# Kernel optimization log

Hardware: AMD Instinct MI355X
Metric: run time of the kernel (lower is better)

## Reference

```python
import jax, jax.numpy as jnp
import numpy as np

LATENT_DIM = 512
IN_CH = 256
OUT_CH = 256
KSIZE = 3
BATCH = 16
RES = 128
SQRT2 = float(np.sqrt(2.0))


def setup_inputs() -> dict:
    key = jax.random.key(0)
    k1, k2, k3, k4, k5 = jax.random.split(key, 5)
    content = jax.random.normal(k1, (BATCH, IN_CH, RES, RES), dtype=jnp.float32)
    latent = jax.random.normal(k2, (BATCH, LATENT_DIM), dtype=jnp.float32)
    noise = jax.random.normal(k3, (BATCH, 1, RES, RES), dtype=jnp.float32)
    # affine: LinearLayer(latentDim, inChannels, doActivation=False), bias filled with 1
    aff_w = jax.random.normal(k4, (IN_CH, LATENT_DIM), dtype=jnp.float32)
    aff_b = jnp.ones((IN_CH,), dtype=jnp.float32)
    conv_w = jax.random.normal(k5, (OUT_CH, IN_CH, KSIZE, KSIZE), dtype=jnp.float32)
    bias = jnp.zeros((1, OUT_CH, 1, 1), dtype=jnp.float32)
    noise_weight = jnp.zeros((), dtype=jnp.float32)
    return {"content": content, "latent": latent, "noise": noise,
            "aff_w": aff_w, "aff_b": aff_b, "conv_w": conv_w,
            "bias": bias, "noise_weight": noise_weight}


def reference(content, latent, noise, aff_w, aff_b, conv_w, bias, noise_weight):
    # affine style: F.linear(latent, W * sqrt(1/latentDim)) + bias (bias init 1, lrMult 1, no act)
    w_mult = np.sqrt(1.0 / aff_w.shape[1]).astype(np.float32)
    style = latent @ (aff_w * w_mult).T + aff_b  # [B, Cin]
    # demodulation factor: d[b,o] = rsqrt(sum_{i,kh,kw} (W[o,i]*style[b,i])^2 + eps)
    w_sq = jnp.sum(conv_w * conv_w, axis=(2, 3))  # [Cout, Cin]
    demod = jax.lax.rsqrt(jnp.einsum('oi,bi->bo', w_sq, style * style) + 1e-8)  # [B, Cout]
    # modulate activations instead of weights (mathematically identical to per-sample grouped conv)
    x = content * style[:, :, None, None]
    pad = KSIZE // 2
    y = jax.lax.conv_general_dilated(
        x, conv_w, window_strides=(1, 1), padding=((pad, pad), (pad, pad)),
        dimension_numbers=('NCHW', 'OIHW', 'NCHW'))
    y = y * demod[:, :, None, None]  # [B, Cout, H, W]
    y = y + noise_weight * noise + bias
    return jax.nn.leaky_relu(y, negative_slope=0.2) * SQRT2
```

## Files before the change

### kernel.cpp

```cpp
#include <hip/hip_runtime.h>


typedef __bf16 bf16;
typedef bf16 bf16x8 __attribute__((ext_vector_type(8)));
typedef bf16 bf16x4 __attribute__((ext_vector_type(4)));
typedef float f32x4 __attribute__((ext_vector_type(4)));

#define GLOBAL_AS __attribute__((address_space(1)))
#define LDS_AS __attribute__((address_space(3)))

__global__ __launch_bounds__(256) void style_k(const float* __restrict__ latent,
                                               const float* __restrict__ aff_w,
                                               const float* __restrict__ aff_b,
                                               float* __restrict__ style) {
  const int wid = blockIdx.x * 4 + (threadIdx.x >> 6);
  const int lane = threadIdx.x & 63;
  const int b = wid >> 8, i = wid & 255;
  float acc = 0.f;
#pragma unroll
  for (int k = 0; k < 8; ++k) {
    const int l = lane + 64 * k;
    acc += latent[b * 512 + l] * aff_w[i * 512 + l];
  }
#pragma unroll
  for (int off = 32; off > 0; off >>= 1) acc += __shfl_xor(acc, off, 64);
  if (lane == 0) style[b * 256 + i] = acc * 0.04419417382415922f + aff_b[i];
}

__global__ __launch_bounds__(256) void demod_k(const float* __restrict__ conv_w,
                                               const float* __restrict__ style,
                                               float* __restrict__ demod) {
  __shared__ float s_wsq[256];
  const int o = blockIdx.x, i = threadIdx.x;
  float wsq = 0.f;
#pragma unroll
  for (int t = 0; t < 9; ++t) {
    const float w = conv_w[(o * 256 + i) * 9 + t];
    wsq += w * w;
  }
  s_wsq[i] = wsq;
  __syncthreads();
  const int wv = threadIdx.x >> 6, lane = threadIdx.x & 63;
  for (int b = wv; b < 16; b += 4) {
    float p = 0.f;
#pragma unroll
    for (int k = 0; k < 4; ++k) {
      const int ii = lane + 64 * k;
      const float s = style[b * 256 + ii];
      p += s_wsq[ii] * s * s;
    }
#pragma unroll
    for (int off = 32; off > 0; off >>= 1) p += __shfl_xor(p, off, 64);
    if (lane == 0) demod[b * 256 + o] = rsqrtf(p + 1e-8f);
  }
}

__global__ __launch_bounds__(256) void wprep_k(const float* __restrict__ conv_w,
                                               bf16* __restrict__ wp) {
  const int idx = blockIdx.x * 256 + threadIdx.x;
  const int ci = idx & 31;
  const int t3 = idx >> 5;
  const int kw = t3 % 3;
  const int t4 = t3 / 3;
  const int m = t4 & 255;
  const int t5 = t4 >> 8;
  const int cc = t5 & 7, kh = t5 >> 3;
  const float v = conv_w[((m * 256 + cc * 32 + ci) * 3 + kh) * 3 + kw];
  wp[idx] = (bf16)v;
}

__global__ __launch_bounds__(1024, 4) void conv_k(const float* __restrict__ content,
                                                  const float* __restrict__ noise,
                                                  const float* __restrict__ bias,
                                                  const float* __restrict__ nwp,
                                                  const float* __restrict__ style,
                                                  const float* __restrict__ demod,
                                                  const bf16* __restrict__ wp,
                                                  float* __restrict__ out) {
  __shared__ __align__(16) char smem[98304 + 41600];
  bf16* ldsA = (bf16*)smem;
  bf16* ldsX = (bf16*)(smem + 98304);

  const int tid = threadIdx.x;
  const int lane = tid & 63, wv = tid >> 6;
  const int bid = blockIdx.x;
  const int sp = ((bid & 7) << 7) | (bid >> 3);
  const int band = sp & 63, b = sp >> 6;
  const int h0 = band * 2;
  const int g = lane >> 4, nl = lane & 15;
  const int m0 = (wv & 3) * 64;
  const int nseg = wv >> 2;
  const int rr = nseg >> 1;
  const int x0 = (nseg & 1) * 64;
  const int wS = tid & 127, grp = tid >> 7;

  f32x4 acc[4][4];
  const f32x4 zero4 = {0.f, 0.f, 0.f, 0.f};
#pragma unroll
  for (int mb = 0; mb < 4; ++mb)
#pragma unroll
    for (int nb = 0; nb < 4; ++nb) acc[mb][nb] = zero4;

  const float* srcb = content + ((size_t)b * 256) * 16384;

  {
#pragma unroll
    for (int i = 0; i < 3; ++i) {
      const int u = tid + i * 1024;
      __builtin_amdgcn_global_load_lds((const GLOBAL_AS void*)(wp + u * 8),
                                       (LDS_AS void*)(ldsA + u * 8), 16, 0, 0);
    }
  }

  int cur = 0;
  for (int cc = 0; cc < 8; ++cc) {
    {
      const int c0 = cc * 32 + grp * 4;
      const float s0 = style[b * 256 + c0 + 0];
      const float s1 = style[b * 256 + c0 + 1];
      const float s2 = style[b * 256 + c0 + 2];
      const float s3 = style[b * 256 + c0 + 3];
#pragma unroll
      for (int r = 0; r < 4; ++r) {
        const int gh = h0 - 1 + r;
        bf16x4 pk = {(bf16)0.f, (bf16)0.f, (bf16)0.f, (bf16)0.f};
        if (gh >= 0 && gh < 128) {
          const float* src = srcb + (size_t)c0 * 16384 + gh * 128 + wS;
          pk[0] = (bf16)(src[0] * s0);
          pk[1] = (bf16)(src[16384] * s1);
          pk[2] = (bf16)(src[2 * 16384] * s2);
          pk[3] = (bf16)(src[3 * 16384] * s3);
        }
        *(bf16x4*)(ldsX + (r * 130 + wS + 1) * 40 + grp * 4) = pk;
      }
      if (tid < 64) {
        const int r = tid >> 4, xh = ((tid >> 3) & 1) ? 129 : 0, q = tid & 7;
        bf16x4 z = {(bf16)0.f, (bf16)0.f, (bf16)0.f, (bf16)0.f};
        *(bf16x4*)(ldsX + (r * 130 + xh) * 40 + q * 4) = z;
      }
    }
    __syncthreads();

    for (int kh = 0; kh < 3; ++kh) {
      const int ncc = (kh == 2) ? cc + 1 : cc;
      const int nkh = (kh == 2) ? 0 : kh + 1;
      if (ncc < 8) {
        const bf16* seg = wp + (size_t)((nkh * 8 + ncc) * 256) * 96;
        bf16* dstA = ldsA + (cur ^ 1) * 24576;
#pragma unroll
        for (int i = 0; i < 3; ++i) {
          const int u = tid + i * 1024;
          __builtin_amdgcn_global_load_lds((const GLOBAL_AS void*)(seg + u * 8),
                                           (LDS_AS void*)(dstA + u * 8), 16, 0, 0);
        }
      }
      const bf16* Abuf = ldsA + cur * 24576;
      const int xrow = rr + kh;
#pragma unroll
      for (int kw = 0; kw < 3; ++kw) {
        bf16x8 af[4], xf[4];
#pragma unroll
        for (int mb = 0; mb < 4; ++mb)
          af[mb] = *(const bf16x8*)(Abuf + (m0 + mb * 16 + nl) * 96 + kw * 32 + g * 8);
#pragma unroll
        for (int nb = 0; nb < 4; ++nb)
          xf[nb] = *(const bf16x8*)(ldsX + (xrow * 130 + x0 + nb * 16 + nl + kw) * 40 + g * 8);
#pragma unroll
        for (int mb = 0; mb < 4; ++mb)
#pragma unroll
          for (int nb = 0; nb < 4; ++nb)
            acc[mb][nb] =
                __builtin_amdgcn_mfma_f32_16x16x32_bf16(af[mb], xf[nb], acc[mb][nb], 0, 0, 0);
      }
      cur ^= 1;
      __syncthreads();
    }
  }

  const float nw = nwp[0];
  const int hr = h0 + rr;
#pragma unroll
  for (int mb = 0; mb < 4; ++mb) {
    const int o = m0 + mb * 16 + g * 4;
    const f32x4 dm = *(const f32x4*)(demod + b * 256 + o);
    const f32x4 bs = *(const f32x4*)(bias + o);
#pragma unroll
    for (int nb = 0; nb < 4; ++nb) {
      const int x = x0 + nb * 16 + nl;
      const float nz = nw * noise[b * 16384 + hr * 128 + x];
      float* op = out + ((size_t)(b * 256 + o)) * 16384 + hr * 128 + x;
#pragma unroll
      for (int r = 0; r < 4; ++r) {
        float y = acc[mb][nb][r] * dm[r] + nz + bs[r];
        y = (y > 0.f ? y : 0.2f * y) * 1.41421356237f;
        op[(size_t)r * 16384] = y;
      }
    }
  }
}

extern "C" void kernel_launch(void* const* d_in, const int* in_sizes, int n_in,
                              void* d_out, int out_size, void* d_ws, size_t ws_size,
                              hipStream_t stream) {
  const float* content = (const float*)d_in[0];
  const float* latent = (const float*)d_in[1];
  const float* noise = (const float*)d_in[2];
  const float* aff_w = (const float*)d_in[3];
  const float* aff_b = (const float*)d_in[4];
  const float* conv_w = (const float*)d_in[5];
  const float* bias = (const float*)d_in[6];
  const float* nw = (const float*)d_in[7];
  float* out = (float*)d_out;

  float* style = (float*)d_ws;
  float* demod = style + 4096;
  bf16* wp = (bf16*)((char*)d_ws + 32768);

  style_k<<<1024, 256, 0, stream>>>(latent, aff_w, aff_b, style);
  demod_k<<<256, 256, 0, stream>>>(conv_w, style, demod);
  wprep_k<<<2304, 256, 0, stream>>>(conv_w, wp);
  conv_k<<<1024, 1024, 0, stream>>>(content, noise, bias, nw, style, demod, wp, out);
}
```

Baseline: 685.6 us.

## Pre-modulate content into swizzled bf16 layout and stream it via direct LDS loads

Adds an xprep kernel that multiplies content by style, converts it to bf16, and writes it to a workspace in a channel-grouped, XOR-swizzled layout. The conv kernel then loads activation tiles with global_load_lds instead of doing strided fp32 loads and conversions inside the main loop. The weight layout is also reorganised so A-fragment reads are contiguous. The costs are an extra full-size pass over content plus a bf16 intermediate in global memory, and the optimised path only runs when the workspace is large enough; otherwise it falls back to the old path with padded LDS rows.

```diff
diff --git a/kernel.cpp b/kernel.cpp
--- a/kernel.cpp
+++ b/kernel.cpp
@@ -58,26 +58,48 @@
 __global__ __launch_bounds__(256) void wprep_k(const float* __restrict__ conv_w,
                                                bf16* __restrict__ wp) {
   const int idx = blockIdx.x * 256 + threadIdx.x;
-  const int ci = idx & 31;
-  const int t3 = idx >> 5;
-  const int kw = t3 % 3;
-  const int t4 = t3 / 3;
-  const int m = t4 & 255;
-  const int t5 = t4 >> 8;
-  const int cc = t5 & 7, kh = t5 >> 3;
-  const float v = conv_w[((m * 256 + cc * 32 + ci) * 3 + kh) * 3 + kw];
-  wp[idx] = (bf16)v;
-}
-
-__global__ __launch_bounds__(1024, 4) void conv_k(const float* __restrict__ content,
+  const int e = idx & 7;
+  const int m = (idx >> 3) & 255;
+  const int g = (idx >> 11) & 3;
+  const int rest = idx >> 13;
+  const int kw = rest % 3;
+  const int t = rest / 3;
+  const int cc = t & 7, kh = t >> 3;
+  wp[idx] = (bf16)conv_w[((m * 256 + cc * 32 + g * 8 + e) * 3 + kh) * 3 + kw];
+}
+
+__global__ __launch_bounds__(256) void xprep_k(const float* __restrict__ content,
+                                               const float* __restrict__ style,
+                                               bf16* __restrict__ xg) {
+  const int blk = blockIdx.x;
+  const int cc = blk & 7, h = (blk >> 3) & 127, b = blk >> 10;
+  const int x = threadIdx.x & 127, gp = threadIdx.x >> 7;
+  bf16* dst = xg + (size_t)blk * 4096;
+#pragma unroll
+  for (int gg = 0; gg < 2; ++gg) {
+    const int g = gp * 2 + gg;
+    const int ci0 = cc * 32 + g * 8;
+    const float* src = content + ((size_t)(b * 256 + ci0)) * 16384 + h * 128 + x;
+    const float* st = style + b * 256 + ci0;
+    bf16x8 v;
+#pragma unroll
+    for (int e = 0; e < 8; ++e) v[e] = (bf16)(src[(size_t)e * 16384] * st[e]);
+    *(bf16x8*)(dst + x * 32 + 8 * ((g + ((x + 1) >> 1)) & 3)) = v;
+  }
+}
+
+template <int XG>
+__global__ __launch_bounds__(1024, 4) void conv_t(const bf16* __restrict__ xg,
+                                                  const float* __restrict__ content,
+                                                  const float* __restrict__ style,
                                                   const float* __restrict__ noise,
                                                   const float* __restrict__ bias,
                                                   const float* __restrict__ nwp,
-                                                  const float* __restrict__ style,
                                                   const float* __restrict__ demod,
                                                   const bf16* __restrict__ wp,
                                                   float* __restrict__ out) {
-  __shared__ __align__(16) char smem[98304 + 41600];
+  constexpr int XROW = XG ? 4160 : 5720;
+  __shared__ __align__(16) char smem[98304 + (XG ? 33280 : 45760)];
   bf16* ldsA = (bf16*)smem;
   bf16* ldsX = (bf16*)(smem + 98304);
 
@@ -92,7 +114,6 @@
   const int nseg = wv >> 2;
   const int rr = nseg >> 1;
   const int x0 = (nseg & 1) * 64;
-  const int wS = tid & 127, grp = tid >> 7;
 
   f32x4 acc[4][4];
   const f32x4 zero4 = {0.f, 0.f, 0.f, 0.f};
@@ -101,29 +122,52 @@
 #pragma unroll
     for (int nb = 0; nb < 4; ++nb) acc[mb][nb] = zero4;
 
-  const float* srcb = content + ((size_t)b * 256) * 16384;
-
-  {
+  const bf16 bz = (bf16)0.f;
+  const bf16x8 z8 = {bz, bz, bz, bz, bz, bz, bz, bz};
+
+  auto stageA = [&](int kh, int cc, int buf) {
+    const bf16* seg = wp + (size_t)(kh * 8 + cc) * 24576;
+    bf16* dstA = ldsA + buf * 24576;
 #pragma unroll
     for (int i = 0; i < 3; ++i) {
       const int u = tid + i * 1024;
-      __builtin_amdgcn_global_load_lds((const GLOBAL_AS void*)(wp + u * 8),
-                                       (LDS_AS void*)(ldsA + u * 8), 16, 0, 0);
-    }
-  }
-
-  int cur = 0;
-  for (int cc = 0; cc < 8; ++cc) {
-    {
+      __builtin_amdgcn_global_load_lds((const GLOBAL_AS void*)(seg + u * 8),
+                                       (LDS_AS void*)(dstA + u * 8), 16, 0, 0);
+    }
+  };
+
+  auto stageX = [&](int cc) {
+    if constexpr (XG) {
+#pragma unroll
+      for (int j = 0; j < 2; ++j) {
+        const int u = tid + j * 1024;
+        const int r = u >> 9;
+        const int gh = h0 - 1 + r;
+        bf16* dst = ldsX + r * XROW + 32 + (u & 511) * 8;
+        if (gh >= 0 && gh < 128) {
+          const bf16* src = xg + (size_t)(((b * 128 + gh) << 3) + cc) * 4096 + (u & 511) * 8;
+          __builtin_amdgcn_global_load_lds((const GLOBAL_AS void*)src, (LDS_AS void*)dst, 16,
+                                           0, 0);
+        } else {
+          *(bf16x8*)dst = z8;
+        }
+      }
+      if (tid < 32) {
+        const int r = tid >> 3, hw = (tid >> 2) & 1, un = tid & 3;
+        *(bf16x8*)(ldsX + r * XROW + (hw ? 4128 : 0) + un * 8) = z8;
+      }
+    } else {
+      const int wS = tid & 127, grp = tid >> 7;
       const int c0 = cc * 32 + grp * 4;
       const float s0 = style[b * 256 + c0 + 0];
       const float s1 = style[b * 256 + c0 + 1];
       const float s2 = style[b * 256 + c0 + 2];
       const float s3 = style[b * 256 + c0 + 3];
+      const float* srcb = content + ((size_t)b * 256) * 16384;
 #pragma unroll
       for (int r = 0; r < 4; ++r) {
         const int gh = h0 - 1 + r;
-        bf16x4 pk = {(bf16)0.f, (bf16)0.f, (bf16)0.f, (bf16)0.f};
+        bf16x4 pk = {bz, bz, bz, bz};
         if (gh >= 0 && gh < 128) {
           const float* src = srcb + (size_t)c0 * 16384 + gh * 128 + wS;
           pk[0] = (bf16)(src[0] * s0);
@@ -131,40 +175,42 @@
           pk[2] = (bf16)(src[2 * 16384] * s2);
           pk[3] = (bf16)(src[3 * 16384] * s3);
         }
-        *(bf16x4*)(ldsX + (r * 130 + wS + 1) * 40 + grp * 4) = pk;
+        *(bf16x4*)(ldsX + (r * 130 + wS + 1) * 44 + grp * 4) = pk;
       }
       if (tid < 64) {
         const int r = tid >> 4, xh = ((tid >> 3) & 1) ? 129 : 0, q = tid & 7;
-        bf16x4 z = {(bf16)0.f, (bf16)0.f, (bf16)0.f, (bf16)0.f};
-        *(bf16x4*)(ldsX + (r * 130 + xh) * 40 + q * 4) = z;
-      }
-    }
-    __syncthreads();
-
+        bf16x4 zz = {bz, bz, bz, bz};
+        *(bf16x4*)(ldsX + (r * 130 + xh) * 44 + q * 4) = zz;
+      }
+    }
+  };
+
+  stageX(0);
+  stageA(0, 0, 0);
+  __syncthreads();
+
+  int cur = 0;
+  for (int cc = 0; cc < 8; ++cc) {
     for (int kh = 0; kh < 3; ++kh) {
       const int ncc = (kh == 2) ? cc + 1 : cc;
       const int nkh = (kh == 2) ? 0 : kh + 1;
-      if (ncc < 8) {
-        const bf16* seg = wp + (size_t)((nkh * 8 + ncc) * 256) * 96;
-        bf16* dstA = ldsA + (cur ^ 1) * 24576;
-#pragma unroll
-        for (int i = 0; i < 3; ++i) {
-          const int u = tid + i * 1024;
-          __builtin_amdgcn_global_load_lds((const GLOBAL_AS void*)(seg + u * 8),
-                                           (LDS_AS void*)(dstA + u * 8), 16, 0, 0);
-        }
-      }
-      const bf16* Abuf = ldsA + cur * 24576;
-      const int xrow = rr + kh;
+      if (ncc < 8) stageA(nkh, ncc, cur ^ 1);
+      const bf16* Ab = ldsA + cur * 24576;
+      const int xr = rr + kh;
 #pragma unroll
       for (int kw = 0; kw < 3; ++kw) {
         bf16x8 af[4], xf[4];
 #pragma unroll
         for (int mb = 0; mb < 4; ++mb)
-          af[mb] = *(const bf16x8*)(Abuf + (m0 + mb * 16 + nl) * 96 + kw * 32 + g * 8);
-#pragma unroll
-        for (int nb = 0; nb < 4; ++nb)
-          xf[nb] = *(const bf16x8*)(ldsX + (xrow * 130 + x0 + nb * 16 + nl + kw) * 40 + g * 8);
+          af[mb] = *(const bf16x8*)(Ab + ((kw * 4 + g) * 256 + m0 + mb * 16 + nl) * 8);
+#pragma unroll
+        for (int nb = 0; nb < 4; ++nb) {
+          const int p1 = x0 + nb * 16 + nl + kw;
+          if constexpr (XG)
+            xf[nb] = *(const bf16x8*)(ldsX + xr * XROW + p1 * 32 + 8 * ((g + (p1 >> 1)) & 3));
+          else
+            xf[nb] = *(const bf16x8*)(ldsX + (xr * 130 + p1) * 44 + g * 8);
+        }
 #pragma unroll
         for (int mb = 0; mb < 4; ++mb)
 #pragma unroll
@@ -173,6 +219,10 @@
                 __builtin_amdgcn_mfma_f32_16x16x32_bf16(af[mb], xf[nb], acc[mb][nb], 0, 0, 0);
       }
       cur ^= 1;
+      __syncthreads();
+    }
+    if (cc < 7) {
+      stageX(cc + 1);
       __syncthreads();
     }
   }
@@ -215,9 +265,17 @@
   float* style = (float*)d_ws;
   float* demod = style + 4096;
   bf16* wp = (bf16*)((char*)d_ws + 32768);
+  bf16* xg = (bf16*)((char*)d_ws + 1212416);
+  const size_t need = 1212416 + (size_t)16384 * 8192;
 
   style_k<<<1024, 256, 0, stream>>>(latent, aff_w, aff_b, style);
   demod_k<<<256, 256, 0, stream>>>(conv_w, style, demod);
   wprep_k<<<2304, 256, 0, stream>>>(conv_w, wp);
-  conv_k<<<1024, 1024, 0, stream>>>(content, noise, bias, nw, style, demod, wp, out);
-}
+  if (ws_size >= need) {
+    xprep_k<<<16384, 256, 0, stream>>>(content, style, xg);
+    conv_t<1><<<1024, 1024, 0, stream>>>(xg, content, style, noise, bias, nw, demod, wp, out);
+  } else {
+    conv_t<0><<<1024, 1024, 0, stream>>>(nullptr, content, style, noise, bias, nw, demod, wp,
+                                         out);
+  }
+}
```

After: 692.0 us. No clear change (+0.9%).
